# Optimization experiments

Measured on AMD Instinct MI355X. Metric: run time of the kernel, lower is better.

Reference implementation:

```python
import jax, jax.numpy as jnp
import numpy as np

B, C_IN, N, T, E, C_OUT = 128, 32, 325, 24, 3, 64


def setup_inputs() -> dict:
    key = jax.random.key(0)
    kx, ka, kw, kb = jax.random.split(key, 4)
    x = jax.random.normal(kx, (B, C_IN, N, T), dtype=jnp.float32)
    supports = jax.random.normal(ka, (E, N, N), dtype=jnp.float32) * (1.0 / np.sqrt(N))
    # 1x1 Conv2d params: weight [c_out, c_in*(edge_dim+1)], bias [c_out]
    fan_in = C_IN * (E + 1)
    W = jax.random.normal(kw, (C_OUT, fan_in), dtype=jnp.float32) * (1.0 / np.sqrt(fan_in))
    b = jax.random.normal(kb, (C_OUT,), dtype=jnp.float32) * 0.05
    return {"x": x, "supports": supports, "W": W, "b": b}


def reference(x, supports, W, b):
    # x: [B, C, N, T], supports: [E, N, N]
    Bb, C, Nn, Tt = x.shape
    # nconv for every support at once: einsum 'bcvt,vw->bcwt' batched over E
    diff = jnp.einsum('bcvt,evw->becwt', x, supports)  # [B, E, C, N, T]
    # concat [x] + diffused copies along channel dim -> [B, (E+1)*C, N, T]
    h = jnp.concatenate([x[:, None], diff], axis=1).reshape(Bb, -1, Nn, Tt)
    # 1x1 conv == channel-mixing matmul; squeeze(-1) is a no-op since T > 1
    out = jnp.einsum('bkvt,ok->bovt', h, W) + b[None, :, None, None]
    return out  # [B, c_out, N, T]
```

## Files before the change

kernel.cpp:

```cpp
#include <hip/hip_runtime.h>
#include <hip/hip_bf16.h>

typedef short bf16x8 __attribute__((ext_vector_type(8)));
typedef float f32x4 __attribute__((ext_vector_type(4)));

static constexpr int Bb   = 128;
static constexpr int Cin  = 32;
static constexpr int Nn   = 325;
static constexpr int Tt   = 24;
static constexpr int Cout = 64;
static constexpr int VP   = 360;
static constexpr int SVP  = 352;
static constexpr int WP   = 336;
static constexpr int NWT  = 21;
static constexpr int NKS  = 11;
static constexpr int TH   = 12;
static constexpr int HPAD = 136;
static constexpr size_t XT_ELEMS  = (size_t)Bb * Tt * Cin * VP;
static constexpr size_t STP_ELEMS = (size_t)4 * WP * SVP;

__global__ void build_stp(const float* __restrict__ sup,
                          __hip_bfloat16* __restrict__ stp) {
    int idx = blockIdx.x * 256 + threadIdx.x;
    int total = 4 * WP * SVP;
    if (idx >= total) return;
    int e = idx / (WP * SVP);
    int r = idx % (WP * SVP);
    int w = r / SVP;
    int v = r % SVP;
    float val = 0.f;
    if (e == 0) {
        val = (v == w && v < Nn) ? 1.f : 0.f;
    } else if (v < Nn && w < Nn) {
        val = sup[((size_t)(e - 1) * Nn + v) * Nn + w];
    }
    stp[idx] = __float2bfloat16(val);
}

__global__ void build_wb(const float* __restrict__ W,
                         __hip_bfloat16* __restrict__ Wb) {
    int i = blockIdx.x * 256 + threadIdx.x;
    if (i < Cout * 128) Wb[i] = __float2bfloat16(W[i]);
}

__global__ void transpose_x(const float* __restrict__ x,
                            __hip_bfloat16* __restrict__ xT) {
    __shared__ float ls[64 * 25];
    int id = blockIdx.x;
    int vt = id % 6;
    int c  = (id / 6) % Cin;
    int b  = id / (6 * Cin);
    int v0 = vt * 64;
    const float* src = x + (size_t)(b * Cin + c) * Nn * Tt;
    for (int i = threadIdx.x; i < 64 * Tt; i += 256) {
        int vi = i / Tt, t = i % Tt;
        int v = v0 + vi;
        ls[vi * 25 + t] = (v < Nn) ? src[(size_t)v * Tt + t] : 0.f;
    }
    __syncthreads();
    for (int j = threadIdx.x; j < 64 * Tt; j += 256) {
        int t = j / 64, vi = j % 64;
        int v = v0 + vi;
        if (v < VP) {
            xT[((size_t)(b * Tt + t) * Cin + c) * VP + v] =
                __float2bfloat16(ls[vi * 25 + t]);
        }
    }
}

__global__ __launch_bounds__(256, 3) void graphconv_main(
    const __hip_bfloat16* __restrict__ xT,
    const __hip_bfloat16* __restrict__ stp,
    const __hip_bfloat16* __restrict__ Wb,
    const float* __restrict__ bias,
    float* __restrict__ out) {
    __shared__ __hip_bfloat16 Hs[192 * HPAD];

    int bid = blockIdx.x;
    int lg  = (bid & 7) * 672 + (bid >> 3);
    int b   = lg / 42;
    int r2  = lg % 42;
    int wt  = r2 >> 1, th = r2 & 1;
    int w0  = wt * 16, t0 = th * TH;

    int tid = threadIdx.x, wid = tid >> 6, lane = tid & 63;
    int cl = lane & 15, kg = lane >> 4, ko8 = kg * 8;

    const __hip_bfloat16* xb = xT + (size_t)(b * Tt + t0) * Cin * VP;
    const __hip_bfloat16* sb = stp + (size_t)(w0 + cl) * SVP + ko8;

    f32x4 acc1[4][6] = {};
    for (int ks = 0; ks < NKS; ++ks) {
        bf16x8 af[4], xf[6];
#pragma unroll
        for (int e = 0; e < 4; ++e)
            af[e] = *(const bf16x8*)(sb + (size_t)e * WP * SVP + ks * 32);
#pragma unroll
        for (int j = 0; j < 6; ++j) {
            int lc = (wid * 6 + j) * 16 + cl;
            xf[j] = *(const bf16x8*)(xb + (size_t)lc * VP + ks * 32 + ko8);
        }
#pragma unroll
        for (int e = 0; e < 4; ++e)
#pragma unroll
            for (int j = 0; j < 6; ++j)
                acc1[e][j] = __builtin_amdgcn_mfma_f32_16x16x32_bf16(
                    af[e], xf[j], acc1[e][j], 0, 0, 0);
    }

#pragma unroll
    for (int e = 0; e < 4; ++e)
#pragma unroll
        for (int j = 0; j < 6; ++j) {
            int lc = (wid * 6 + j) * 16 + cl;
            int tl = lc >> 5, c = lc & 31;
#pragma unroll
            for (int r = 0; r < 4; ++r) {
                int n = (kg * 4 + r) * TH + tl;
                Hs[n * HPAD + e * 32 + c] = __float2bfloat16(acc1[e][j][r]);
            }
        }
    __syncthreads();

    f32x4 acc2[4][3] = {};
#pragma unroll
    for (int ks2 = 0; ks2 < 4; ++ks2) {
        bf16x8 wf[4], hf[3];
#pragma unroll
        for (int mt = 0; mt < 4; ++mt)
            wf[mt] = *(const bf16x8*)(Wb + (mt * 16 + cl) * 128 + ks2 * 32 + ko8);
#pragma unroll
        for (int nt = 0; nt < 3; ++nt)
            hf[nt] = *(const bf16x8*)&Hs[((wid * 3 + nt) * 16 + cl) * HPAD + ks2 * 32 + ko8];
#pragma unroll
        for (int mt = 0; mt < 4; ++mt)
#pragma unroll
            for (int nt = 0; nt < 3; ++nt)
                acc2[mt][nt] = __builtin_amdgcn_mfma_f32_16x16x32_bf16(
                    wf[mt], hf[nt], acc2[mt][nt], 0, 0, 0);
    }

#pragma unroll
    for (int nt = 0; nt < 3; ++nt) {
        int n = (wid * 3 + nt) * 16 + cl;
        int wl = n / TH, tl = n - wl * TH;
        int w = w0 + wl;
        if (w < Nn) {
#pragma unroll
            for (int mt = 0; mt < 4; ++mt) {
                int o = mt * 16 + kg * 4;
                size_t base = ((size_t)(b * Cout + o) * Nn + w) * Tt + t0 + tl;
#pragma unroll
                for (int r = 0; r < 4; ++r)
                    out[base + (size_t)r * Nn * Tt] = acc2[mt][nt][r] + bias[o + r];
            }
        }
    }
}

extern "C" void kernel_launch(void* const* d_in, const int* in_sizes, int n_in,
                              void* d_out, int out_size, void* d_ws, size_t ws_size,
                              hipStream_t stream) {
    const float* x    = (const float*)d_in[0];
    const float* sup  = (const float*)d_in[1];
    const float* W    = (const float*)d_in[2];
    const float* bias = (const float*)d_in[3];
    float* out = (float*)d_out;

    __hip_bfloat16* xT  = (__hip_bfloat16*)d_ws;
    __hip_bfloat16* stp = xT + XT_ELEMS;
    __hip_bfloat16* Wb  = stp + STP_ELEMS;

    build_stp<<<(int)((STP_ELEMS + 255) / 256), 256, 0, stream>>>(sup, stp);
    build_wb<<<(Cout * 128 + 255) / 256, 256, 0, stream>>>(W, Wb);
    transpose_x<<<Bb * Cin * 6, 256, 0, stream>>>(x, xT);
    graphconv_main<<<Bb * NWT * 2, 256, 0, stream>>>(xT, stp, Wb, bias, out);
}
```

Baseline: 345.6 us.

## Stage X and supports through double-buffered LDS and fuse second GEMM in registers

The main kernel now loads X and support tiles into double-buffered, XOR-swizzled LDS using global_load_lds, prefetching the next K-slice while the current one computes. The second (1x1 conv) GEMM reads the first GEMM's accumulators directly from registers via 16x16x16 MFMAs, which removes the Hs shared-memory round trip. W is converted to bf16 inside the kernel, so the separate build_wb launch is dropped. Occupancy is lowered to 2 blocks per SM to fit the larger LDS footprint. Each block also redoes the W conversion, which adds some redundant work.

```diff
diff --git a/kernel.cpp b/kernel.cpp
--- a/kernel.cpp
+++ b/kernel.cpp
@@ -2,7 +2,8 @@
 #include <hip/hip_bf16.h>
 
 typedef short bf16x8 __attribute__((ext_vector_type(8)));
-typedef float f32x4 __attribute__((ext_vector_type(4)));
+typedef short bf16x4 __attribute__((ext_vector_type(4)));
+typedef float f32x4  __attribute__((ext_vector_type(4)));
 
 static constexpr int Bb   = 128;
 static constexpr int Cin  = 32;
@@ -15,9 +16,18 @@
 static constexpr int NWT  = 21;
 static constexpr int NKS  = 11;
 static constexpr int TH   = 12;
-static constexpr int HPAD = 136;
 static constexpr size_t XT_ELEMS  = (size_t)Bb * Tt * Cin * VP;
 static constexpr size_t STP_ELEMS = (size_t)4 * WP * SVP;
+
+__device__ __forceinline__ void gld16(const void* g, void* l) {
+    __builtin_amdgcn_global_load_lds(
+        (const __attribute__((address_space(1))) void*)g,
+        (__attribute__((address_space(3))) void*)l, 16, 0, 0);
+}
+__device__ __forceinline__ short bfb(float f) {
+    __hip_bfloat16 h = __float2bfloat16(f);
+    return *reinterpret_cast<short*>(&h);
+}
 
 __global__ void build_stp(const float* __restrict__ sup,
                           __hip_bfloat16* __restrict__ stp) {
@@ -37,12 +47,6 @@
     stp[idx] = __float2bfloat16(val);
 }
 
-__global__ void build_wb(const float* __restrict__ W,
-                         __hip_bfloat16* __restrict__ Wb) {
-    int i = blockIdx.x * 256 + threadIdx.x;
-    if (i < Cout * 128) Wb[i] = __float2bfloat16(W[i]);
-}
-
 __global__ void transpose_x(const float* __restrict__ x,
                             __hip_bfloat16* __restrict__ xT) {
     __shared__ float ls[64 * 25];
@@ -68,13 +72,16 @@
     }
 }
 
-__global__ __launch_bounds__(256, 3) void graphconv_main(
+__global__ __launch_bounds__(256, 2) void graphconv_main(
     const __hip_bfloat16* __restrict__ xT,
     const __hip_bfloat16* __restrict__ stp,
-    const __hip_bfloat16* __restrict__ Wb,
+    const float* __restrict__ W,
     const float* __restrict__ bias,
     float* __restrict__ out) {
-    __shared__ __hip_bfloat16 Hs[192 * HPAD];
+    __shared__ alignas(16) __hip_bfloat16 Xs[2][384 * 32];
+    __shared__ alignas(16) __hip_bfloat16 Ss[2][64 * 32];
+    __shared__ alignas(16) __hip_bfloat16 Ws[64 * 128];
+    __shared__ float bias_s[Cout];
 
     int bid = blockIdx.x;
     int lg  = (bid & 7) * 672 + (bid >> 3);
@@ -84,75 +91,98 @@
     int w0  = wt * 16, t0 = th * TH;
 
     int tid = threadIdx.x, wid = tid >> 6, lane = tid & 63;
-    int cl = lane & 15, kg = lane >> 4, ko8 = kg * 8;
-
-    const __hip_bfloat16* xb = xT + (size_t)(b * Tt + t0) * Cin * VP;
-    const __hip_bfloat16* sb = stp + (size_t)(w0 + cl) * SVP + ko8;
+    int cl = lane & 15, kg = lane >> 4;
+
+    int srow   = lane >> 2;
+    int sslotB = (((lane & 3) ^ ((lane >> 3) & 3)) << 4);
+    int xsw = ((kg ^ ((cl >> 1) & 3)) << 4);
+
+    const char* xb = (const char*)(xT + (size_t)(b * Tt + t0) * Cin * VP);
+    const char* sb = (const char*)stp;
+
+    for (int c2 = tid; c2 < 2048; c2 += 256) {
+        int row = c2 >> 5, s = c2 & 31;
+        const float* wp = W + (size_t)c2 * 4;
+        bf16x4 pk = { bfb(wp[0]), bfb(wp[1]), bfb(wp[2]), bfb(wp[3]) };
+        *(bf16x4*)((char*)Ws + row * 256 + ((s ^ (row & 15)) << 3)) = pk;
+    }
+    if (tid < Cout) bias_s[tid] = bias[tid];
+
+#pragma unroll
+    for (int ii = 0; ii < 6; ++ii) {
+        int chunk = wid * 6 + ii;
+        gld16(xb + (size_t)(chunk * 16 + srow) * (VP * 2) + sslotB,
+              (char*)&Xs[0][0] + chunk * 1024 + lane * 16);
+    }
+    gld16(sb + ((size_t)(wid * WP + w0 + srow) * SVP) * 2 + sslotB,
+          (char*)&Ss[0][0] + wid * 1024 + lane * 16);
+    __syncthreads();
 
     f32x4 acc1[4][6] = {};
+    int bb = 0;
     for (int ks = 0; ks < NKS; ++ks) {
-        bf16x8 af[4], xf[6];
+        if (ks + 1 < NKS) {
+#pragma unroll
+            for (int ii = 0; ii < 6; ++ii) {
+                int chunk = wid * 6 + ii;
+                gld16(xb + (size_t)(chunk * 16 + srow) * (VP * 2) + (ks + 1) * 64 + sslotB,
+                      (char*)&Xs[bb ^ 1][0] + chunk * 1024 + lane * 16);
+            }
+            gld16(sb + ((size_t)(wid * WP + w0 + srow) * SVP) * 2 + (ks + 1) * 64 + sslotB,
+                  (char*)&Ss[bb ^ 1][0] + wid * 1024 + lane * 16);
+        }
+        bf16x8 xf[6], af[4];
+#pragma unroll
+        for (int j = 0; j < 6; ++j)
+            xf[j] = *(const bf16x8*)((const char*)&Xs[bb][0] +
+                                     (((wid * 6 + j) * 16 + cl) << 6) + xsw);
 #pragma unroll
         for (int e = 0; e < 4; ++e)
-            af[e] = *(const bf16x8*)(sb + (size_t)e * WP * SVP + ks * 32);
-#pragma unroll
-        for (int j = 0; j < 6; ++j) {
-            int lc = (wid * 6 + j) * 16 + cl;
-            xf[j] = *(const bf16x8*)(xb + (size_t)lc * VP + ks * 32 + ko8);
-        }
+            af[e] = *(const bf16x8*)((const char*)&Ss[bb][0] +
+                                     (((e * 16 + cl) << 6)) + xsw);
 #pragma unroll
         for (int e = 0; e < 4; ++e)
 #pragma unroll
             for (int j = 0; j < 6; ++j)
                 acc1[e][j] = __builtin_amdgcn_mfma_f32_16x16x32_bf16(
-                    af[e], xf[j], acc1[e][j], 0, 0, 0);
-    }
-
-#pragma unroll
-    for (int e = 0; e < 4; ++e)
-#pragma unroll
-        for (int j = 0; j < 6; ++j) {
-            int lc = (wid * 6 + j) * 16 + cl;
-            int tl = lc >> 5, c = lc & 31;
+                    xf[j], af[e], acc1[e][j], 0, 0, 0);
+        __syncthreads();
+        bb ^= 1;
+    }
+
+    f32x4 acc2[4][3] = {};
+#pragma unroll
+    for (int kappa = 0; kappa < 8; ++kappa) {
+        int e = kappa >> 1, half = kappa & 1;
+        bf16x4 wf[4];
+#pragma unroll
+        for (int mt = 0; mt < 4; ++mt)
+            wf[mt] = *(const bf16x4*)((const char*)Ws + (mt * 16 + cl) * 256 +
+                                      ((((kappa * 4 + kg) ^ cl)) << 3));
+#pragma unroll
+        for (int tj = 0; tj < 3; ++tj) {
+            int j = tj * 2 + half;
+            f32x4 y = acc1[e][j];
+            bf16x4 pb = { bfb(y[0]), bfb(y[1]), bfb(y[2]), bfb(y[3]) };
+#pragma unroll
+            for (int mt = 0; mt < 4; ++mt)
+                acc2[mt][tj] = __builtin_amdgcn_mfma_f32_16x16x16bf16_1k(
+                    wf[mt], pb, acc2[mt][tj], 0, 0, 0);
+        }
+    }
+
+    int w = w0 + cl;
+    if (w < Nn) {
+#pragma unroll
+        for (int mt = 0; mt < 4; ++mt) {
 #pragma unroll
             for (int r = 0; r < 4; ++r) {
-                int n = (kg * 4 + r) * TH + tl;
-                Hs[n * HPAD + e * 32 + c] = __float2bfloat16(acc1[e][j][r]);
-            }
-        }
-    __syncthreads();
-
-    f32x4 acc2[4][3] = {};
-#pragma unroll
-    for (int ks2 = 0; ks2 < 4; ++ks2) {
-        bf16x8 wf[4], hf[3];
-#pragma unroll
-        for (int mt = 0; mt < 4; ++mt)
-            wf[mt] = *(const bf16x8*)(Wb + (mt * 16 + cl) * 128 + ks2 * 32 + ko8);
-#pragma unroll
-        for (int nt = 0; nt < 3; ++nt)
-            hf[nt] = *(const bf16x8*)&Hs[((wid * 3 + nt) * 16 + cl) * HPAD + ks2 * 32 + ko8];
-#pragma unroll
-        for (int mt = 0; mt < 4; ++mt)
-#pragma unroll
-            for (int nt = 0; nt < 3; ++nt)
-                acc2[mt][nt] = __builtin_amdgcn_mfma_f32_16x16x32_bf16(
-                    wf[mt], hf[nt], acc2[mt][nt], 0, 0, 0);
-    }
-
-#pragma unroll
-    for (int nt = 0; nt < 3; ++nt) {
-        int n = (wid * 3 + nt) * 16 + cl;
-        int wl = n / TH, tl = n - wl * TH;
-        int w = w0 + wl;
-        if (w < Nn) {
-#pragma unroll
-            for (int mt = 0; mt < 4; ++mt) {
-                int o = mt * 16 + kg * 4;
-                size_t base = ((size_t)(b * Cout + o) * Nn + w) * Tt + t0 + tl;
-#pragma unroll
-                for (int r = 0; r < 4; ++r)
-                    out[base + (size_t)r * Nn * Tt] = acc2[mt][nt][r] + bias[o + r];
+                int o = mt * 16 + kg * 4 + r;
+                size_t base = ((size_t)(b * Cout + o) * Nn + w) * Tt + t0 + wid * 3;
+                float bv = bias_s[o];
+#pragma unroll
+                for (int tj = 0; tj < 3; ++tj)
+                    out[base + tj] = acc2[mt][tj][r] + bv;
             }
         }
     }
@@ -169,10 +199,8 @@
 
     __hip_bfloat16* xT  = (__hip_bfloat16*)d_ws;
     __hip_bfloat16* stp = xT + XT_ELEMS;
-    __hip_bfloat16* Wb  = stp + STP_ELEMS;
 
     build_stp<<<(int)((STP_ELEMS + 255) / 256), 256, 0, stream>>>(sup, stp);
-    build_wb<<<(Cout * 128 + 255) / 256, 256, 0, stream>>>(W, Wb);
     transpose_x<<<Bb * Cin * 6, 256, 0, stream>>>(x, xT);
-    graphconv_main<<<Bb * NWT * 2, 256, 0, stream>>>(xT, stp, Wb, bias, out);
-}
+    graphconv_main<<<Bb * NWT * 2, 256, 0, stream>>>(xT, stp, W, bias, out);
+}
```

Measured after the change: 353.7 us. +2.4%, slower.
